# Kernel optimization log

Measured on AMD Instinct MI355X. Metric: run time of the kernel, lower is better.

The kernel has to match this reference:

```python
import jax, jax.numpy as jnp
import numpy as np
import math

D_MODEL = 512
N_HEADS = 8
D_K = D_MODEL // N_HEADS
N_SAMPLES = 16
BETA = 1.0
SCALE = 1.0 / math.sqrt(D_K)
PROPOSAL_TEMP = 0.5


def setup_inputs() -> dict:
    key = jax.random.key(0)
    ks = jax.random.split(key, 9)
    B, S = 2, 512
    x = jax.random.normal(ks[0], (B, S, D_MODEL), dtype=jnp.float32)
    init = lambda k: jax.random.normal(k, (D_MODEL, D_MODEL), dtype=jnp.float32) * 0.02
    return {
        "x": x,
        "Wq": init(ks[1]), "bq": jnp.zeros((D_MODEL,), jnp.float32),
        "Wk": init(ks[2]), "bk": jnp.zeros((D_MODEL,), jnp.float32),
        "Wv": init(ks[3]), "bv": jnp.zeros((D_MODEL,), jnp.float32),
        "Wo": init(ks[4]), "bo": jnp.zeros((D_MODEL,), jnp.float32),
    }


def _importance_sampled_weights(scores):
    # scores: [B,H,S,S]. Replicates the per-row Python loop, fully vectorized.
    B, H, Sq, Sk = scores.shape
    target = jax.nn.softmax(scores * BETA, axis=-1)            # [B,H,Sq,Sk]
    # optimal proposal: 0.5*target + 0.5*uniform
    prop = PROPOSAL_TEMP * target + (1.0 - PROPOSAL_TEMP) / Sk
    R = B * H * Sq
    tf = target.reshape(R, Sk)
    pf = prop.reshape(R, Sk)
    # tsu_backend.sample_binary_layer(log(p/(1-p))) == Bernoulli(p) sampling
    s = jax.random.bernoulli(jax.random.key(42), pf[:, None, :], (R, N_SAMPLES, Sk))
    # importance weight = prod(target[sel]) / (prod(prop[sel]) * prod(1-prop[~sel]))
    pt = jnp.prod(jnp.where(s, tf[:, None, :], 1.0), axis=-1)                 # [R,N]
    pp = jnp.prod(jnp.where(s, pf[:, None, :], 1.0 - pf[:, None, :]), axis=-1)
    valid = (s.sum(-1) > 0) & (pp > 0)
    w = jnp.where(valid, pt / jnp.maximum(pp, 1e-38), 0.0)
    ws = w.sum(-1, keepdims=True)
    w = jnp.where(ws > 0, w / jnp.maximum(ws, 1e-38), 1.0 / N_SAMPLES)        # [R,N]
    wa = jnp.einsum('rn,rnk->rk', w, s.astype(jnp.float32))                   # [R,Sk]
    was = wa.sum(-1, keepdims=True)
    wa = jnp.where(was > 0, wa / jnp.maximum(was, 1e-38), 1.0 / Sk)
    return wa.reshape(B, H, Sq, Sk)


def reference(x, Wq, bq, Wk, bk, Wv, bv, Wo, bo):
    B, S, Dm = x.shape
    proj = lambda W, b: (x @ W + b).reshape(B, S, N_HEADS, D_K).transpose(0, 2, 1, 3)
    Q = proj(Wq, bq)  # [B,H,S,dk]
    K = proj(Wk, bk)
    V = proj(Wv, bv)
    scores = jnp.einsum('bhqd,bhkd->bhqk', Q, K) * SCALE
    # torch builds weights via torch.tensor(...) which detaches => constant w.r.t. params
    attn = jax.lax.stop_gradient(_importance_sampled_weights(scores))
    out = jnp.einsum('bhqk,bhkd->bhqd', attn, V)
    out = out.transpose(0, 2, 1, 3).reshape(B, S, Dm)
    return out @ Wo + bo
```

## Files before the change

### kernel.cpp

```cpp
#include <hip/hip_runtime.h>
#include <cstdint>
#include <cstddef>


#if __has_builtin(__builtin_amdgcn_alignbit)
#define ROTL(x, r) __builtin_amdgcn_alignbit((x), (x), 32 - (r))
#else
#define ROTL(x, r) (((x) << (r)) | ((x) >> (32 - (r))))
#endif

#define QR8(s)                                                                \
  x0[0]+=x1[0];x0[1]+=x1[1];x0[2]+=x1[2];x0[3]+=x1[3];                        \
  x0[4]+=x1[4];x0[5]+=x1[5];x0[6]+=x1[6];x0[7]+=x1[7];                        \
  x1[0]=ROTL(x1[0],s);x1[1]=ROTL(x1[1],s);x1[2]=ROTL(x1[2],s);                \
  x1[3]=ROTL(x1[3],s);x1[4]=ROTL(x1[4],s);x1[5]=ROTL(x1[5],s);                \
  x1[6]=ROTL(x1[6],s);x1[7]=ROTL(x1[7],s);                                    \
  x1[0]^=x0[0];x1[1]^=x0[1];x1[2]^=x0[2];x1[3]^=x0[3];                        \
  x1[4]^=x0[4];x1[5]^=x0[5];x1[6]^=x0[6];x1[7]^=x0[7];
#define INJ8(X, Y)                                                            \
  x0[0]+=(X);x0[1]+=(X);x0[2]+=(X);x0[3]+=(X);                                \
  x0[4]+=(X);x0[5]+=(X);x0[6]+=(X);x0[7]+=(X);                                \
  x1[0]+=(Y);x1[1]+=(Y);x1[2]+=(Y);x1[3]+=(Y);                                \
  x1[4]+=(Y);x1[5]+=(Y);x1[6]+=(Y);x1[7]+=(Y);
#define INJ8Y(Y)                                                              \
  x1[0]+=(Y);x1[1]+=(Y);x1[2]+=(Y);x1[3]+=(Y);                                \
  x1[4]+=(Y);x1[5]+=(Y);x1[6]+=(Y);x1[7]+=(Y);

__global__ __launch_bounds__(256)
void qkv_gemm(const float* __restrict__ x,
              const float* __restrict__ Wq, const float* __restrict__ bq,
              const float* __restrict__ Wk, const float* __restrict__ bk,
              const float* __restrict__ Wv, const float* __restrict__ bv,
              float* __restrict__ Qw, float* __restrict__ KTw,
              float* __restrict__ Vw) {
  const float* W; const float* bias; float* out;
  if (blockIdx.z == 0)      { W = Wq; bias = bq; out = Qw; }
  else if (blockIdx.z == 1) { W = Wk; bias = bk; out = KTw; }
  else                      { W = Wv; bias = bv; out = Vw; }

  __shared__ float At[32][68];
  __shared__ float Bs[32][64];
  const int tid = threadIdx.x;
  const int tx = tid & 15, ty = tid >> 4;
  const int row0 = blockIdx.x * 64, col0 = blockIdx.y * 64;
  float acc[4][4] = {};

  for (int kk = 0; kk < 512; kk += 32) {
    const int ar = tid >> 2;
#pragma unroll
    for (int i = 0; i < 2; ++i) {
      const int kc = ((tid & 3) << 3) + (i << 2);
      const float4 a4 =
          *(const float4*)&x[(size_t)(row0 + ar) * 512 + kk + kc];
      At[kc + 0][ar] = a4.x; At[kc + 1][ar] = a4.y;
      At[kc + 2][ar] = a4.z; At[kc + 3][ar] = a4.w;
    }
#pragma unroll
    for (int i = 0; i < 2; ++i) {
      const int idx = tid + (i << 8);
      const int br = idx >> 4, bc = (idx & 15) << 2;
      *(float4*)&Bs[br][bc] =
          *(const float4*)&W[(size_t)(kk + br) * 512 + col0 + bc];
    }
    __syncthreads();
#pragma unroll
    for (int p = 0; p < 32; ++p) {
      const float4 a4 = *(const float4*)&At[p][ty << 2];
      const float4 b4 = *(const float4*)&Bs[p][tx << 2];
      acc[0][0] = fmaf(a4.x, b4.x, acc[0][0]); acc[0][1] = fmaf(a4.x, b4.y, acc[0][1]);
      acc[0][2] = fmaf(a4.x, b4.z, acc[0][2]); acc[0][3] = fmaf(a4.x, b4.w, acc[0][3]);
      acc[1][0] = fmaf(a4.y, b4.x, acc[1][0]); acc[1][1] = fmaf(a4.y, b4.y, acc[1][1]);
      acc[1][2] = fmaf(a4.y, b4.z, acc[1][2]); acc[1][3] = fmaf(a4.y, b4.w, acc[1][3]);
      acc[2][0] = fmaf(a4.z, b4.x, acc[2][0]); acc[2][1] = fmaf(a4.z, b4.y, acc[2][1]);
      acc[2][2] = fmaf(a4.z, b4.z, acc[2][2]); acc[2][3] = fmaf(a4.z, b4.w, acc[2][3]);
      acc[3][0] = fmaf(a4.w, b4.x, acc[3][0]); acc[3][1] = fmaf(a4.w, b4.y, acc[3][1]);
      acc[3][2] = fmaf(a4.w, b4.z, acc[3][2]); acc[3][3] = fmaf(a4.w, b4.w, acc[3][3]);
    }
    __syncthreads();
  }
  const bool isK = (blockIdx.z == 1);
#pragma unroll
  for (int i = 0; i < 4; ++i) {
    const int row = row0 + (ty << 2) + i;
    const int b = row >> 9, s = row & 511;
#pragma unroll
    for (int j = 0; j < 4; ++j) {
      const int col = col0 + (tx << 2) + j;
      const int h = col >> 6, d = col & 63;
      const float v = acc[i][j] + bias[col];
      if (isK)
        out[(((size_t)(b * 8 + h) * 64 + d) * 512) + s] = v;
      else
        out[(((size_t)(b * 8 + h) * 512 + s) * 64) + d] = v;
    }
  }
}

__global__ __launch_bounds__(256)
void out_gemm(const float* __restrict__ A, const float* __restrict__ W,
              const float* __restrict__ bias, float* __restrict__ C) {
  __shared__ float At[32][68];
  __shared__ float Bs[32][64];
  const int tid = threadIdx.x;
  const int tx = tid & 15, ty = tid >> 4;
  const int row0 = blockIdx.x * 64, col0 = blockIdx.y * 64;
  float acc[4][4] = {};

  for (int kk = 0; kk < 512; kk += 32) {
    const int ar = tid >> 2;
#pragma unroll
    for (int i = 0; i < 2; ++i) {
      const int kc = ((tid & 3) << 3) + (i << 2);
      const float4 a4 =
          *(const float4*)&A[(size_t)(row0 + ar) * 512 + kk + kc];
      At[kc + 0][ar] = a4.x; At[kc + 1][ar] = a4.y;
      At[kc + 2][ar] = a4.z; At[kc + 3][ar] = a4.w;
    }
#pragma unroll
    for (int i = 0; i < 2; ++i) {
      const int idx = tid + (i << 8);
      const int br = idx >> 4, bc = (idx & 15) << 2;
      *(float4*)&Bs[br][bc] =
          *(const float4*)&W[(size_t)(kk + br) * 512 + col0 + bc];
    }
    __syncthreads();
#pragma unroll
    for (int p = 0; p < 32; ++p) {
      const float4 a4 = *(const float4*)&At[p][ty << 2];
      const float4 b4 = *(const float4*)&Bs[p][tx << 2];
      acc[0][0] = fmaf(a4.x, b4.x, acc[0][0]); acc[0][1] = fmaf(a4.x, b4.y, acc[0][1]);
      acc[0][2] = fmaf(a4.x, b4.z, acc[0][2]); acc[0][3] = fmaf(a4.x, b4.w, acc[0][3]);
      acc[1][0] = fmaf(a4.y, b4.x, acc[1][0]); acc[1][1] = fmaf(a4.y, b4.y, acc[1][1]);
      acc[1][2] = fmaf(a4.y, b4.z, acc[1][2]); acc[1][3] = fmaf(a4.y, b4.w, acc[1][3]);
      acc[2][0] = fmaf(a4.z, b4.x, acc[2][0]); acc[2][1] = fmaf(a4.z, b4.y, acc[2][1]);
      acc[2][2] = fmaf(a4.z, b4.z, acc[2][2]); acc[2][3] = fmaf(a4.z, b4.w, acc[2][3]);
      acc[3][0] = fmaf(a4.w, b4.x, acc[3][0]); acc[3][1] = fmaf(a4.w, b4.y, acc[3][1]);
      acc[3][2] = fmaf(a4.w, b4.z, acc[3][2]); acc[3][3] = fmaf(a4.w, b4.w, acc[3][3]);
    }
    __syncthreads();
  }
#pragma unroll
  for (int i = 0; i < 4; ++i) {
    const int row = row0 + (ty << 2) + i;
#pragma unroll
    for (int j = 0; j < 4; ++j) {
      const int col = col0 + (tx << 2) + j;
      C[(size_t)row * 512 + col] = acc[i][j] + bias[col];
    }
  }
}

__global__ __launch_bounds__(256)
void scores_softmax(const float* __restrict__ Q, const float* __restrict__ KT,
                    float* __restrict__ tf_g) {
  const int blk = blockIdx.x;
  const int bh = blk >> 7, q0 = (blk & 127) << 2;
  const int tid = threadIdx.x;
  __shared__ __align__(16) float qs[4][64];
  __shared__ __align__(16) float Ks[16][512];
  __shared__ float redm[4][4], reds[4][4];
  qs[tid >> 6][tid & 63] =
      Q[((size_t)bh * 512 + q0 + (tid >> 6)) * 64 + (tid & 63)];

  float a[4][2] = {};
  const float* KTb = KT + (size_t)bh * 64 * 512;
  for (int c = 0; c < 4; ++c) {
    __syncthreads();
#pragma unroll
    for (int i = 0; i < 8; ++i) {
      const int slot = tid + (i << 8);
      const int dr = slot >> 7, dc = (slot & 127) << 2;
      *(float4*)&Ks[dr][dc] =
          *(const float4*)&KTb[(size_t)(c * 16 + dr) * 512 + dc];
    }
    __syncthreads();
#pragma unroll
    for (int ii = 0; ii < 2; ++ii) {
      const int k = tid + (ii << 8);
#pragma unroll
      for (int d4 = 0; d4 < 4; ++d4) {
        const float k0 = Ks[d4 * 4 + 0][k];
        const float k1 = Ks[d4 * 4 + 1][k];
        const float k2 = Ks[d4 * 4 + 2][k];
        const float k3 = Ks[d4 * 4 + 3][k];
        const float4 v0 = ((const float4*)qs[0])[c * 4 + d4];
        const float4 v1 = ((const float4*)qs[1])[c * 4 + d4];
        const float4 v2 = ((const float4*)qs[2])[c * 4 + d4];
        const float4 v3 = ((const float4*)qs[3])[c * 4 + d4];
        a[0][ii] = fmaf(v0.x, k0, a[0][ii]); a[0][ii] = fmaf(v0.y, k1, a[0][ii]);
        a[0][ii] = fmaf(v0.z, k2, a[0][ii]); a[0][ii] = fmaf(v0.w, k3, a[0][ii]);
        a[1][ii] = fmaf(v1.x, k0, a[1][ii]); a[1][ii] = fmaf(v1.y, k1, a[1][ii]);
        a[1][ii] = fmaf(v1.z, k2, a[1][ii]); a[1][ii] = fmaf(v1.w, k3, a[1][ii]);
        a[2][ii] = fmaf(v2.x, k0, a[2][ii]); a[2][ii] = fmaf(v2.y, k1, a[2][ii]);
        a[2][ii] = fmaf(v2.z, k2, a[2][ii]); a[2][ii] = fmaf(v2.w, k3, a[2][ii]);
        a[3][ii] = fmaf(v3.x, k0, a[3][ii]); a[3][ii] = fmaf(v3.y, k1, a[3][ii]);
        a[3][ii] = fmaf(v3.z, k2, a[3][ii]); a[3][ii] = fmaf(v3.w, k3, a[3][ii]);
      }
    }
  }
  float sc[4][2];
#pragma unroll
  for (int i = 0; i < 4; ++i) {
    sc[i][0] = a[i][0] * 0.125f;
    sc[i][1] = a[i][1] * 0.125f;
  }
  float mx[4];
#pragma unroll
  for (int i = 0; i < 4; ++i) mx[i] = fmaxf(sc[i][0], sc[i][1]);
  for (int m = 1; m < 64; m <<= 1) {
#pragma unroll
    for (int i = 0; i < 4; ++i) mx[i] = fmaxf(mx[i], __shfl_xor(mx[i], m));
  }
  if ((tid & 63) == 0) {
    const int w = tid >> 6;
#pragma unroll
    for (int i = 0; i < 4; ++i) redm[i][w] = mx[i];
  }
  __syncthreads();
  float ex[4][2], sm[4];
#pragma unroll
  for (int i = 0; i < 4; ++i) {
    const float rm = fmaxf(fmaxf(redm[i][0], redm[i][1]),
                           fmaxf(redm[i][2], redm[i][3]));
    ex[i][0] = expf(sc[i][0] - rm);
    ex[i][1] = expf(sc[i][1] - rm);
    sm[i] = ex[i][0] + ex[i][1];
  }
  for (int m = 1; m < 64; m <<= 1) {
#pragma unroll
    for (int i = 0; i < 4; ++i) sm[i] += __shfl_xor(sm[i], m);
  }
  if ((tid & 63) == 0) {
    const int w = tid >> 6;
#pragma unroll
    for (int i = 0; i < 4; ++i) reds[i][w] = sm[i];
  }
  __syncthreads();
#pragma unroll
  for (int i = 0; i < 4; ++i) {
    const float tot = reds[i][0] + reds[i][1] + reds[i][2] + reds[i][3];
    tf_g[((size_t)bh * 512 + q0 + i) * 512 + tid]       = ex[i][0] / tot;
    tf_g[((size_t)bh * 512 + q0 + i) * 512 + tid + 256] = ex[i][1] / tot;
  }
}

__global__ __launch_bounds__(256)
void sample_attnv(const float* __restrict__ tf_g, const float* __restrict__ V,
                  float* __restrict__ ao) {
  const int r = blockIdx.x;
  const int b = r >> 12, h = (r >> 9) & 7, q = r & 511;
  const int tid = threadIdx.x;
  __shared__ float tf[512];
  __shared__ __align__(16) uint32_t pscu2[512];
  __shared__ float wa[512];
  __shared__ float wr[16];
  __shared__ float redc[8];
  __shared__ float psum[4][64];
  __shared__ int   list[512];
  __shared__ int   cnt;

  if (tid == 0) cnt = 0;
  {
    const float t0 = tf_g[(size_t)r * 512 + tid];
    const float t1 = tf_g[(size_t)r * 512 + tid + 256];
    tf[tid] = t0; tf[tid + 256] = t1;
    wa[tid] = 0.f; wa[tid + 256] = 0.f;
    const float p0 = fmaf(0.5f, t0, 0.0009765625f);
    const float p1 = fmaf(0.5f, t1, 0.0009765625f);
    {
      const int k = tid;
      pscu2[(((k & 31) >> 2) << 6) + ((k >> 5) << 2) + (k & 3)] =
          ((uint32_t)ceilf(p0 * 8388608.0f)) << 9;
    }
    {
      const int k = tid + 256;
      pscu2[(((k & 31) >> 2) << 6) + ((k >> 5) << 2) + (k & 3)] =
          ((uint32_t)ceilf(p1 * 8388608.0f)) << 9;
    }
    float ql = (1.f - p0) * (1.f - p1);
    for (int m = 1; m < 64; m <<= 1) ql *= __shfl_xor(ql, m);
    if ((tid & 63) == 0) redc[4 + (tid >> 6)] = ql;
  }
  __syncthreads();
  const float Qrow = redc[4] * redc[5] * redc[6] * redc[7];

  const int n = tid >> 4, t = tid & 15;
  const int k0 = t << 5;
  const uint32_t cbase =
      (uint32_t)r * 8192u + (uint32_t)n * 512u + (uint32_t)k0 + 42u;
  uint32_t bits = 0u;
#pragma unroll
  for (int jb = 0; jb < 32; jb += 8) {
    uint32_t x0[8], x1[8];
#pragma unroll
    for (int i = 0; i < 8; ++i) { x0[i] = 0u; x1[i] = cbase + (uint32_t)(jb + i); }
    QR8(13) QR8(15) QR8(26) QR8(6)
    INJ8(42u, 0x1BD11BF1u)
    QR8(17) QR8(29) QR8(16) QR8(24)
    INJ8(0x1BD11BF0u, 2u)
    QR8(13) QR8(15) QR8(26) QR8(6)
    INJ8Y(45u)
    QR8(17) QR8(29) QR8(16) QR8(24)
    INJ8(42u, 0x1BD11BF4u)
    QR8(13) QR8(15) QR8(26) QR8(6)
    INJ8(0x1BD11BF0u, 5u)
    const uint4 pA = *(const uint4*)&pscu2[((jb >> 2) << 6) + (t << 2)];
    const uint4 pB = *(const uint4*)&pscu2[(((jb >> 2) + 1) << 6) + (t << 2)];
    bits |= (uint32_t)((x0[0] ^ x1[0]) < pA.x) << (jb + 0);
    bits |= (uint32_t)((x0[1] ^ x1[1]) < pA.y) << (jb + 1);
    bits |= (uint32_t)((x0[2] ^ x1[2]) < pA.z) << (jb + 2);
    bits |= (uint32_t)((x0[3] ^ x1[3]) < pA.w) << (jb + 3);
    bits |= (uint32_t)((x0[4] ^ x1[4]) < pB.x) << (jb + 4);
    bits |= (uint32_t)((x0[5] ^ x1[5]) < pB.y) << (jb + 5);
    bits |= (uint32_t)((x0[6] ^ x1[6]) < pB.z) << (jb + 6);
    bits |= (uint32_t)((x0[7] ^ x1[7]) < pB.w) << (jb + 7);
  }

  float ptl = 1.f, ratl = 1.f;
  int cl = __popc(bits);
  {
    uint32_t bb = bits;
    while (bb) {
      const int j = __builtin_ctz(bb);
      bb &= bb - 1u;
      const float tv = tf[k0 + j];
      const float p = fmaf(0.5f, tv, 0.0009765625f);
      ptl *= tv;
      ratl *= p / (1.f - p);
    }
  }
#pragma unroll
  for (int m = 1; m < 16; m <<= 1) {
    ptl *= __shfl_xor(ptl, m);
    ratl *= __shfl_xor(ratl, m);
    cl += __shfl_xor(cl, m);
  }
  if (t == 0) {
    const float pp = Qrow * ratl;
    wr[n] = (cl > 0 && pp > 0.f) ? (ptl / fmaxf(pp, 1e-38f)) : 0.f;
  }
  __syncthreads();
  float wsum = 0.f;
#pragma unroll
  for (int m2 = 0; m2 < 16; ++m2) wsum += wr[m2];
  const float wn = (wsum > 0.f) ? (wr[n] / fmaxf(wsum, 1e-38f)) : 0.0625f;
  {
    uint32_t bb = bits;
    while (bb) {
      const int j = __builtin_ctz(bb);
      bb &= bb - 1u;
      atomicAdd(&wa[k0 + j], wn);
    }
  }
  __syncthreads();

  float sp = wa[tid] + wa[tid + 256];
  for (int m = 1; m < 64; m <<= 1) sp += __shfl_xor(sp, m);
  if ((tid & 63) == 0) redc[tid >> 6] = sp;
  if (wa[tid] > 0.f)       { const int i = atomicAdd(&cnt, 1); list[i] = tid; }
  if (wa[tid + 256] > 0.f) { const int i = atomicAdd(&cnt, 1); list[i] = tid + 256; }
  __syncthreads();
  const float was = redc[0] + redc[1] + redc[2] + redc[3];
  const int nnz = cnt;

  const int g = tid >> 6, d = tid & 63;
  const float* Vb = V + ((size_t)(b * 8 + h) * 512) * 64;
  float acc = 0.f;
  if (was > 0.f) {
    const float inv = 1.f / fmaxf(was, 1e-38f);
    for (int i = g; i < nnz; i += 4) {
      const int k = list[i];
      acc = fmaf(wa[k] * inv, Vb[(size_t)k * 64 + d], acc);
    }
  } else {
    for (int k = g; k < 512; k += 4) acc += Vb[(size_t)k * 64 + d];
    acc *= 0.001953125f;
  }
  psum[g][d] = acc;
  __syncthreads();
  if (g == 0) {
    ao[((size_t)(b * 512 + q) * 512) + h * 64 + d] =
        psum[0][d] + psum[1][d] + psum[2][d] + psum[3][d];
  }
}

extern "C" void kernel_launch(void* const* d_in, const int* in_sizes, int n_in,
                              void* d_out, int out_size, void* d_ws,
                              size_t ws_size, hipStream_t stream) {
  const float* x  = (const float*)d_in[0];
  const float* Wq = (const float*)d_in[1];
  const float* bq = (const float*)d_in[2];
  const float* Wk = (const float*)d_in[3];
  const float* bk = (const float*)d_in[4];
  const float* Wv = (const float*)d_in[5];
  const float* bv = (const float*)d_in[6];
  const float* Wo = (const float*)d_in[7];
  const float* bo = (const float*)d_in[8];
  float* out = (float*)d_out;

  float* ws = (float*)d_ws;
  float* Qw = ws;
  float* KT = ws + 524288;
  float* Vw = ws + 1048576;
  float* tf = ws + 1572864;
  float* ao = ws + 5767168;

  dim3 gq(16, 8, 3);
  qkv_gemm<<<gq, 256, 0, stream>>>(x, Wq, bq, Wk, bk, Wv, bv, Qw, KT, Vw);
  scores_softmax<<<2048, 256, 0, stream>>>(Qw, KT, tf);
  sample_attnv<<<8192, 256, 0, stream>>>(tf, Vw, ao);
  dim3 go(16, 8);
  out_gemm<<<go, 256, 0, stream>>>(ao, Wo, bo, out);
}
```

Before: 284.9 us.

## Coalesce K-transpose stores, read K directly, and peel first Threefry round

The QKV GEMM now stages the K tile through shared memory so the transposed K^T output is written with contiguous float4 stores instead of strided scalar stores. The scores kernel drops its 32 KB shared K staging and its per-chunk barriers, reading K^T straight from global memory (coalesced across threads), which frees LDS and should raise occupancy. The first Threefry round is folded algebraically because x0 starts at zero, and the rotate uses a generic builtin. The risk is more global load traffic in the scores kernel, which now relies on cache hits instead of explicit LDS reuse.

```diff
diff --git a/kernel.cpp b/kernel.cpp
--- a/kernel.cpp
+++ b/kernel.cpp
@@ -3,11 +3,7 @@
 #include <cstddef>
 
 
-#if __has_builtin(__builtin_amdgcn_alignbit)
-#define ROTL(x, r) __builtin_amdgcn_alignbit((x), (x), 32 - (r))
-#else
-#define ROTL(x, r) (((x) << (r)) | ((x) >> (32 - (r))))
-#endif
+#define ROTL(x, r) __builtin_rotateleft32((x), (r))
 
 #define QR8(s)                                                                \
   x0[0]+=x1[0];x0[1]+=x1[1];x0[2]+=x1[2];x0[3]+=x1[3];                        \
@@ -40,6 +36,7 @@
 
   __shared__ float At[32][68];
   __shared__ float Bs[32][64];
+  __shared__ __align__(16) float T2[64][68];
   const int tid = threadIdx.x;
   const int tx = tid & 15, ty = tid >> 4;
   const int row0 = blockIdx.x * 64, col0 = blockIdx.y * 64;
@@ -78,20 +75,36 @@
     }
     __syncthreads();
   }
-  const bool isK = (blockIdx.z == 1);
-#pragma unroll
-  for (int i = 0; i < 4; ++i) {
-    const int row = row0 + (ty << 2) + i;
-    const int b = row >> 9, s = row & 511;
-#pragma unroll
-    for (int j = 0; j < 4; ++j) {
-      const int col = col0 + (tx << 2) + j;
-      const int h = col >> 6, d = col & 63;
-      const float v = acc[i][j] + bias[col];
-      if (isK)
-        out[(((size_t)(b * 8 + h) * 64 + d) * 512) + s] = v;
-      else
-        out[(((size_t)(b * 8 + h) * 512 + s) * 64) + d] = v;
+  if (blockIdx.z == 1) {
+#pragma unroll
+    for (int i = 0; i < 4; ++i) {
+#pragma unroll
+      for (int j = 0; j < 4; ++j) {
+        const int col = col0 + (tx << 2) + j;
+        T2[(tx << 2) + j][(ty << 2) + i] = acc[i][j] + bias[col];
+      }
+    }
+    __syncthreads();
+    const int c = tid >> 2, seg = tid & 3;
+    const int b = row0 >> 9, h = col0 >> 6;
+    const int s0 = (row0 & 511) + (seg << 4);
+    float* dst = KTw + (((size_t)(b * 8 + h) * 64 + c) << 9) + s0;
+#pragma unroll
+    for (int i2 = 0; i2 < 4; ++i2) {
+      const float4 v4 = *(const float4*)&T2[c][(seg << 4) + (i2 << 2)];
+      *(float4*)&dst[i2 << 2] = v4;
+    }
+  } else {
+#pragma unroll
+    for (int i = 0; i < 4; ++i) {
+      const int row = row0 + (ty << 2) + i;
+      const int b = row >> 9, s = row & 511;
+#pragma unroll
+      for (int j = 0; j < 4; ++j) {
+        const int col = col0 + (tx << 2) + j;
+        const int h = col >> 6, d = col & 63;
+        out[(((size_t)(b * 8 + h) * 512 + s) * 64) + d] = acc[i][j] + bias[col];
+      }
     }
   }
 }
@@ -157,52 +170,38 @@
   const int bh = blk >> 7, q0 = (blk & 127) << 2;
   const int tid = threadIdx.x;
   __shared__ __align__(16) float qs[4][64];
-  __shared__ __align__(16) float Ks[16][512];
   __shared__ float redm[4][4], reds[4][4];
   qs[tid >> 6][tid & 63] =
       Q[((size_t)bh * 512 + q0 + (tid >> 6)) * 64 + (tid & 63)];
-
-  float a[4][2] = {};
-  const float* KTb = KT + (size_t)bh * 64 * 512;
-  for (int c = 0; c < 4; ++c) {
-    __syncthreads();
-#pragma unroll
-    for (int i = 0; i < 8; ++i) {
-      const int slot = tid + (i << 8);
-      const int dr = slot >> 7, dc = (slot & 127) << 2;
-      *(float4*)&Ks[dr][dc] =
-          *(const float4*)&KTb[(size_t)(c * 16 + dr) * 512 + dc];
-    }
-    __syncthreads();
-#pragma unroll
-    for (int ii = 0; ii < 2; ++ii) {
-      const int k = tid + (ii << 8);
-#pragma unroll
-      for (int d4 = 0; d4 < 4; ++d4) {
-        const float k0 = Ks[d4 * 4 + 0][k];
-        const float k1 = Ks[d4 * 4 + 1][k];
-        const float k2 = Ks[d4 * 4 + 2][k];
-        const float k3 = Ks[d4 * 4 + 3][k];
-        const float4 v0 = ((const float4*)qs[0])[c * 4 + d4];
-        const float4 v1 = ((const float4*)qs[1])[c * 4 + d4];
-        const float4 v2 = ((const float4*)qs[2])[c * 4 + d4];
-        const float4 v3 = ((const float4*)qs[3])[c * 4 + d4];
-        a[0][ii] = fmaf(v0.x, k0, a[0][ii]); a[0][ii] = fmaf(v0.y, k1, a[0][ii]);
-        a[0][ii] = fmaf(v0.z, k2, a[0][ii]); a[0][ii] = fmaf(v0.w, k3, a[0][ii]);
-        a[1][ii] = fmaf(v1.x, k0, a[1][ii]); a[1][ii] = fmaf(v1.y, k1, a[1][ii]);
-        a[1][ii] = fmaf(v1.z, k2, a[1][ii]); a[1][ii] = fmaf(v1.w, k3, a[1][ii]);
-        a[2][ii] = fmaf(v2.x, k0, a[2][ii]); a[2][ii] = fmaf(v2.y, k1, a[2][ii]);
-        a[2][ii] = fmaf(v2.z, k2, a[2][ii]); a[2][ii] = fmaf(v2.w, k3, a[2][ii]);
-        a[3][ii] = fmaf(v3.x, k0, a[3][ii]); a[3][ii] = fmaf(v3.y, k1, a[3][ii]);
-        a[3][ii] = fmaf(v3.z, k2, a[3][ii]); a[3][ii] = fmaf(v3.w, k3, a[3][ii]);
-      }
-    }
-  }
+  __syncthreads();
+
   float sc[4][2];
 #pragma unroll
-  for (int i = 0; i < 4; ++i) {
-    sc[i][0] = a[i][0] * 0.125f;
-    sc[i][1] = a[i][1] * 0.125f;
+  for (int ii = 0; ii < 2; ++ii) {
+    const int k = tid + ii * 256;
+    const float* Kp = KT + (size_t)bh * 64 * 512 + k;
+    float a0 = 0.f, a1 = 0.f, a2 = 0.f, a3 = 0.f;
+#pragma unroll
+    for (int d4 = 0; d4 < 16; ++d4) {
+      const float4 v0 = ((const float4*)qs[0])[d4];
+      const float4 v1 = ((const float4*)qs[1])[d4];
+      const float4 v2 = ((const float4*)qs[2])[d4];
+      const float4 v3 = ((const float4*)qs[3])[d4];
+      const float k0 = Kp[(size_t)(d4 * 4 + 0) * 512];
+      const float k1 = Kp[(size_t)(d4 * 4 + 1) * 512];
+      const float k2 = Kp[(size_t)(d4 * 4 + 2) * 512];
+      const float k3 = Kp[(size_t)(d4 * 4 + 3) * 512];
+      a0 = fmaf(v0.x, k0, a0); a0 = fmaf(v0.y, k1, a0);
+      a0 = fmaf(v0.z, k2, a0); a0 = fmaf(v0.w, k3, a0);
+      a1 = fmaf(v1.x, k0, a1); a1 = fmaf(v1.y, k1, a1);
+      a1 = fmaf(v1.z, k2, a1); a1 = fmaf(v1.w, k3, a1);
+      a2 = fmaf(v2.x, k0, a2); a2 = fmaf(v2.y, k1, a2);
+      a2 = fmaf(v2.z, k2, a2); a2 = fmaf(v2.w, k3, a2);
+      a3 = fmaf(v3.x, k0, a3); a3 = fmaf(v3.y, k1, a3);
+      a3 = fmaf(v3.z, k2, a3); a3 = fmaf(v3.w, k3, a3);
+    }
+    sc[0][ii] = a0 * 0.125f; sc[1][ii] = a1 * 0.125f;
+    sc[2][ii] = a2 * 0.125f; sc[3][ii] = a3 * 0.125f;
   }
   float mx[4];
 #pragma unroll
@@ -293,8 +292,12 @@
   for (int jb = 0; jb < 32; jb += 8) {
     uint32_t x0[8], x1[8];
 #pragma unroll
-    for (int i = 0; i < 8; ++i) { x0[i] = 0u; x1[i] = cbase + (uint32_t)(jb + i); }
-    QR8(13) QR8(15) QR8(26) QR8(6)
+    for (int i = 0; i < 8; ++i) {
+      const uint32_t c = cbase + (uint32_t)(jb + i);
+      x0[i] = c;
+      x1[i] = ROTL(c, 13) ^ c;
+    }
+    QR8(15) QR8(26) QR8(6)
     INJ8(42u, 0x1BD11BF1u)
     QR8(17) QR8(29) QR8(16) QR8(24)
     INJ8(0x1BD11BF0u, 2u)
```

Result: faster. 276.9 us (-2.8%).
